# Kernel tuning notes

Measured on AMD Instinct MI355X. Metric: run time of the kernel, lower is better.

The kernel has to match this reference:

```python
import jax, jax.numpy as jnp
import numpy as np

ALPHA = 0.01  # LeakyReLU negative slope
NEG_INF = -1e12

def setup_inputs() -> dict:
    key = jax.random.key(0)
    k1, k2, k3, k4 = jax.random.split(key, 4)
    B, N, F_in, F_out = 8, 2048, 256, 128
    inp = jax.random.normal(k1, (B, N, F_in), dtype=jnp.float32)
    adj = jax.random.randint(k2, (B, N, N), 0, 2, dtype=jnp.int32)
    # xavier_uniform with gain=1.414
    limW = 1.414 * np.sqrt(6.0 / (F_in + F_out))
    W = jax.random.uniform(k3, (F_in, F_out), minval=-limW, maxval=limW, dtype=jnp.float32)
    lima = 1.414 * np.sqrt(6.0 / (2 * F_out + 1))
    a = jax.random.uniform(k4, (2 * F_out, 1), minval=-lima, maxval=lima, dtype=jnp.float32)
    return {"inp": inp, "adj": adj, "W": W, "a": a}

def reference(inp, adj, W, a):
    # h: [B, N, F_out]
    h = jnp.matmul(inp, W)
    F_out = W.shape[1]
    # Algebraic split of the attention vector: a = [a1; a2], so
    # e[b,i,j] = leakyrelu(h_i . a1 + h_j . a2)  -- avoids the O(N^2*2F) a_input.
    a1 = a[:F_out, 0]   # [F_out]
    a2 = a[F_out:, 0]   # [F_out]
    s1 = jnp.einsum('bnf,f->bn', h, a1)  # [B, N] source term
    s2 = jnp.einsum('bnf,f->bn', h, a2)  # [B, N] target term
    e = s1[:, :, None] + s2[:, None, :]  # [B, N, N]
    e = jnp.where(e > 0, e, ALPHA * e)   # leaky relu
    scores = jnp.where(adj > 0, e, NEG_INF)
    attention = jax.nn.softmax(scores, axis=2)  # [B, N, N]
    h_prime = jnp.matmul(attention, h)          # [B, N, F_out]
    return jax.nn.relu(h_prime)  # concat=True branch
```

## Files before the change

### kernel.cpp

```cpp
#include <hip/hip_runtime.h>
#include <hip/hip_bf16.h>

#define N_    2048
#define FIN   256
#define FOUT  128
#define ALPHA 0.01f
#define NEGINF -1000000000000.0f

typedef short bf16x8 __attribute__((ext_vector_type(8)));
typedef float f32x4  __attribute__((ext_vector_type(4)));

static __device__ __forceinline__ unsigned short f2bf(float x) {
    __hip_bfloat16 h = __float2bfloat16(x);
    return *reinterpret_cast<unsigned short*>(&h);
}

__global__ __launch_bounds__(256) void k_lin(
    const float* __restrict__ inp, const float* __restrict__ W,
    const float* __restrict__ av, __hip_bfloat16* __restrict__ hT,
    float* __restrict__ s1, float* __restrict__ s2)
{
    __shared__ float in_lds[32 * FIN];
    int g = blockIdx.x;
    int b = g & 7;
    int tile = g >> 3;
    int i0 = tile << 5;
    int t = threadIdx.x;

    const float4* src = reinterpret_cast<const float4*>(inp + ((size_t)(b * N_ + i0)) * FIN);
    float4* dst = reinterpret_cast<float4*>(in_lds);
#pragma unroll
    for (int c = 0; c < 8; ++c) dst[t + 256 * c] = src[t + 256 * c];
    __syncthreads();

    int fq = t & 31;
    int rg = t >> 5;
    float acc[4][4];
#pragma unroll
    for (int r = 0; r < 4; ++r)
#pragma unroll
        for (int j = 0; j < 4; ++j) acc[r][j] = 0.f;

    const float4* W4 = reinterpret_cast<const float4*>(W);
    for (int k = 0; k < FIN; k += 4) {
        float4 inr[4];
#pragma unroll
        for (int r = 0; r < 4; ++r)
            inr[r] = *reinterpret_cast<const float4*>(&in_lds[(rg * 4 + r) * FIN + k]);
#pragma unroll
        for (int kk = 0; kk < 4; ++kk) {
            float4 w4 = W4[(k + kk) * 32 + fq];
#pragma unroll
            for (int r = 0; r < 4; ++r) {
                float iv = (&inr[r].x)[kk];
                acc[r][0] = fmaf(iv, w4.x, acc[r][0]);
                acc[r][1] = fmaf(iv, w4.y, acc[r][1]);
                acc[r][2] = fmaf(iv, w4.z, acc[r][2]);
                acc[r][3] = fmaf(iv, w4.w, acc[r][3]);
            }
        }
    }

    float a1v[4], a2v[4];
#pragma unroll
    for (int j = 0; j < 4; ++j) {
        a1v[j] = av[fq * 4 + j];
        a2v[j] = av[FOUT + fq * 4 + j];
    }
#pragma unroll
    for (int r = 0; r < 4; ++r) {
        float p1 = acc[r][0] * a1v[0] + acc[r][1] * a1v[1] + acc[r][2] * a1v[2] + acc[r][3] * a1v[3];
        float p2 = acc[r][0] * a2v[0] + acc[r][1] * a2v[1] + acc[r][2] * a2v[2] + acc[r][3] * a2v[3];
#pragma unroll
        for (int off = 1; off < 32; off <<= 1) {
            p1 += __shfl_xor(p1, off);
            p2 += __shfl_xor(p2, off);
        }
        if (fq == 0) {
            int row = i0 + rg * 4 + r;
            s1[b * N_ + row] = p1;
            s2[b * N_ + row] = p2;
        }
    }

#pragma unroll
    for (int j = 0; j < 4; ++j) {
        ushort4 pk;
        pk.x = f2bf(acc[0][j]);
        pk.y = f2bf(acc[1][j]);
        pk.z = f2bf(acc[2][j]);
        pk.w = f2bf(acc[3][j]);
        *reinterpret_cast<ushort4*>(
            &hT[((size_t)(b * FOUT + fq * 4 + j)) * N_ + i0 + rg * 4]) = pk;
    }
}

__global__ __launch_bounds__(256, 4) void k_attn(
    const int* __restrict__ adj, const __hip_bfloat16* __restrict__ hT,
    const float* __restrict__ s1g, const float* __restrict__ s2g,
    float* __restrict__ out)
{
    __shared__ float m_s[4][16];
    __shared__ float l_s[4][16];
    __shared__ float L_s[16];
    __shared__ float accb[4][16][132];

    int g = blockIdx.x;
    int b = g & 7;
    int tile = g >> 3;
    int i0 = tile << 4;
    int t = threadIdx.x;
    int w = t >> 6;
    int l = t & 63;
    int r = l & 15;
    int lg = l >> 4;
    int jc = w * 512;

    const float s1r = s1g[b * N_ + i0 + r];
    size_t adj_off = ((size_t)(b * N_ + i0 + r)) * N_ + jc + lg * 8;
    const int4*   adjp = reinterpret_cast<const int4*>(adj + adj_off);
    const float4* s2p  = reinterpret_cast<const float4*>(s2g + b * N_ + jc + lg * 8);
    const bf16x8* hv   = reinterpret_cast<const bf16x8*>(hT);
    size_t h0 = (((size_t)(b * FOUT + r)) * N_ + jc + lg * 8) >> 3;
    const size_t FRAG_STRIDE = (size_t)16 * N_ / 8;

    float m_run = -3.0e38f;
    float l_run = 0.0f;
    f32x4 acc[8];
#pragma unroll
    for (int q = 0; q < 8; ++q) acc[q] = (f32x4){0.f, 0.f, 0.f, 0.f};

    for (int step = 0; step < 16; ++step) {
        int4 aj0 = adjp[step * 8];
        int4 aj1 = adjp[step * 8 + 1];
        float4 s2a = s2p[step * 8];
        float4 s2b = s2p[step * 8 + 1];

        float ev[8];
        ev[0] = s1r + s2a.x; ev[1] = s1r + s2a.y; ev[2] = s1r + s2a.z; ev[3] = s1r + s2a.w;
        ev[4] = s1r + s2b.x; ev[5] = s1r + s2b.y; ev[6] = s1r + s2b.z; ev[7] = s1r + s2b.w;
        int aji[8] = {aj0.x, aj0.y, aj0.z, aj0.w, aj1.x, aj1.y, aj1.z, aj1.w};
#pragma unroll
        for (int e = 0; e < 8; ++e) {
            float v = ev[e];
            v = fmaxf(v, ALPHA * v);
            ev[e] = (aji[e] > 0) ? v : NEGINF;
        }
        float mt = fmaxf(fmaxf(fmaxf(ev[0], ev[1]), fmaxf(ev[2], ev[3])),
                         fmaxf(fmaxf(ev[4], ev[5]), fmaxf(ev[6], ev[7])));
        mt = fmaxf(mt, __shfl_xor(mt, 16));
        mt = fmaxf(mt, __shfl_xor(mt, 32));

        if (__any(mt > m_run)) {
            float sc = (mt > m_run) ? __expf(m_run - mt) : 1.0f;
            m_run = fmaxf(m_run, mt);
            l_run *= sc;
            float sr0 = __shfl(sc, lg * 4 + 0);
            float sr1 = __shfl(sc, lg * 4 + 1);
            float sr2 = __shfl(sc, lg * 4 + 2);
            float sr3 = __shfl(sc, lg * 4 + 3);
            f32x4 srv = (f32x4){sr0, sr1, sr2, sr3};
#pragma unroll
            for (int q = 0; q < 8; ++q) acc[q] *= srv;
        }

        bf16x8 af;
        float ps = 0.f;
#pragma unroll
        for (int e = 0; e < 8; ++e) {
            float p = __expf(ev[e] - m_run);
            ps += p;
            af[e] = (short)f2bf(p);
        }
        l_run += ps;

#pragma unroll
        for (int q = 0; q < 8; ++q) {
            bf16x8 bfr = hv[h0 + (size_t)q * FRAG_STRIDE + step * 4];
            acc[q] = __builtin_amdgcn_mfma_f32_16x16x32_bf16(af, bfr, acc[q], 0, 0, 0);
        }
    }

    l_run += __shfl_xor(l_run, 16);
    l_run += __shfl_xor(l_run, 32);
    if (l < 16) { m_s[w][l] = m_run; l_s[w][l] = l_run; }
    __syncthreads();

    float mysc[4];
#pragma unroll
    for (int rr = 0; rr < 4; ++rr) {
        int ir = lg * 4 + rr;
        float M = fmaxf(fmaxf(m_s[0][ir], m_s[1][ir]), fmaxf(m_s[2][ir], m_s[3][ir]));
        float Ls = l_s[0][ir] * __expf(m_s[0][ir] - M)
                 + l_s[1][ir] * __expf(m_s[1][ir] - M)
                 + l_s[2][ir] * __expf(m_s[2][ir] - M)
                 + l_s[3][ir] * __expf(m_s[3][ir] - M);
        mysc[rr] = __expf(m_s[w][ir] - M);
        if (w == 0 && r == 0) L_s[ir] = Ls;
    }
#pragma unroll
    for (int q = 0; q < 8; ++q)
#pragma unroll
        for (int rr = 0; rr < 4; ++rr)
            accb[w][lg * 4 + rr][q * 16 + r] = acc[q][rr] * mysc[rr];
    __syncthreads();

    int f = t & 127;
    int rh = t >> 7;
#pragma unroll
    for (int rr = 0; rr < 8; ++rr) {
        int row = rh * 8 + rr;
        float v = accb[0][row][f] + accb[1][row][f] + accb[2][row][f] + accb[3][row][f];
        v = v / L_s[row];
        out[((size_t)(b * N_ + i0 + row)) * FOUT + f] = fmaxf(v, 0.f);
    }
}

extern "C" void kernel_launch(void* const* d_in, const int* in_sizes, int n_in,
                              void* d_out, int out_size, void* d_ws, size_t ws_size,
                              hipStream_t stream) {
    (void)in_sizes; (void)n_in; (void)out_size; (void)ws_size;
    const float* inp = (const float*)d_in[0];
    const int*   adj = (const int*)d_in[1];
    const float* W   = (const float*)d_in[2];
    const float* a   = (const float*)d_in[3];
    float* out = (float*)d_out;

    char* ws = (char*)d_ws;
    __hip_bfloat16* hT = (__hip_bfloat16*)ws;
    float* s1 = (float*)(ws + (size_t)8 * FOUT * N_ * 2);
    float* s2 = s1 + 8 * N_;

    k_lin<<<512, 256, 0, stream>>>(inp, W, a, hT, s1, s2);
    k_attn<<<1024, 256, 0, stream>>>(adj, hT, s1, s2, out);
}
```

Baseline: 284.4 us.

## Use precomputed per-row softmax bound instead of online max rescaling

Adds a small kernel that computes the per-batch maximum of s2. Because LeakyReLU is monotonic, leakyrelu(s1_i + max s2) bounds every score in row i, so the attention kernel drops the online max tracking, the accumulator rescaling and the cross-wave max merge. It also prefetches the next step's adj and s2 registers, and stages hT stores through LDS so the global writes are coalesced 32-byte chunks. The risk is accuracy: if the bound sits far above a row's real masked maximum, the exponentials can underflow. It also adds one extra kernel launch.

Result: no change. 286.6 us (+0.8%).

```diff
diff --git a/kernel.cpp b/kernel.cpp
--- a/kernel.cpp
+++ b/kernel.cpp
@@ -5,7 +5,6 @@
 #define FIN   256
 #define FOUT  128
 #define ALPHA 0.01f
-#define NEGINF -1000000000000.0f
 
 typedef short bf16x8 __attribute__((ext_vector_type(8)));
 typedef float f32x4  __attribute__((ext_vector_type(4)));
@@ -83,27 +82,49 @@
         }
     }
 
-#pragma unroll
-    for (int j = 0; j < 4; ++j) {
-        ushort4 pk;
-        pk.x = f2bf(acc[0][j]);
-        pk.y = f2bf(acc[1][j]);
-        pk.z = f2bf(acc[2][j]);
-        pk.w = f2bf(acc[3][j]);
-        *reinterpret_cast<ushort4*>(
-            &hT[((size_t)(b * FOUT + fq * 4 + j)) * N_ + i0 + rg * 4]) = pk;
-    }
+    __syncthreads();
+    unsigned short* hb = reinterpret_cast<unsigned short*>(in_lds);
+#pragma unroll
+    for (int j = 0; j < 4; ++j)
+#pragma unroll
+        for (int r = 0; r < 4; ++r)
+            hb[(fq * 4 + j) * 33 + rg * 4 + r] = f2bf(acc[r][j]);
+    __syncthreads();
+    {
+        int f = t >> 1;
+        int c0 = (t & 1) * 16;
+        unsigned short tmp[16];
+#pragma unroll
+        for (int c = 0; c < 16; ++c) tmp[c] = hb[f * 33 + c0 + c];
+        int4* dst4 = reinterpret_cast<int4*>(&hT[((size_t)(b * FOUT + f)) * N_ + i0 + c0]);
+        dst4[0] = reinterpret_cast<const int4*>(tmp)[0];
+        dst4[1] = reinterpret_cast<const int4*>(tmp)[1];
+    }
+}
+
+__global__ __launch_bounds__(256) void k_s2max(const float* __restrict__ s2,
+                                               float* __restrict__ s2max)
+{
+    __shared__ float red[4];
+    int b = blockIdx.x, t = threadIdx.x;
+    const float4* p = reinterpret_cast<const float4*>(s2 + b * N_);
+    float4 v0 = p[t], v1 = p[t + 256];
+    float m = fmaxf(fmaxf(fmaxf(v0.x, v0.y), fmaxf(v0.z, v0.w)),
+                    fmaxf(fmaxf(v1.x, v1.y), fmaxf(v1.z, v1.w)));
+#pragma unroll
+    for (int off = 1; off < 64; off <<= 1) m = fmaxf(m, __shfl_xor(m, off));
+    if ((t & 63) == 0) red[t >> 6] = m;
+    __syncthreads();
+    if (t == 0) s2max[b] = fmaxf(fmaxf(red[0], red[1]), fmaxf(red[2], red[3]));
 }
 
 __global__ __launch_bounds__(256, 4) void k_attn(
     const int* __restrict__ adj, const __hip_bfloat16* __restrict__ hT,
     const float* __restrict__ s1g, const float* __restrict__ s2g,
-    float* __restrict__ out)
+    const float* __restrict__ s2maxg, float* __restrict__ out)
 {
-    __shared__ float m_s[4][16];
+    __shared__ float accb[4][16][128];
     __shared__ float l_s[4][16];
-    __shared__ float L_s[16];
-    __shared__ float accb[4][16][132];
 
     int g = blockIdx.x;
     int b = g & 7;
@@ -117,58 +138,43 @@
     int jc = w * 512;
 
     const float s1r = s1g[b * N_ + i0 + r];
-    size_t adj_off = ((size_t)(b * N_ + i0 + r)) * N_ + jc + lg * 8;
-    const int4*   adjp = reinterpret_cast<const int4*>(adj + adj_off);
-    const float4* s2p  = reinterpret_cast<const float4*>(s2g + b * N_ + jc + lg * 8);
-    const bf16x8* hv   = reinterpret_cast<const bf16x8*>(hT);
+    float eb = s1r + s2maxg[b];
+    const float m_row = fmaxf(eb, ALPHA * eb);
+
+    const int4* adjp = reinterpret_cast<const int4*>(
+        adj + ((size_t)(b * N_ + i0 + r)) * N_ + jc + lg * 8);
+    const float4* s2p = reinterpret_cast<const float4*>(s2g + b * N_ + jc + lg * 8);
+    const bf16x8* hv = reinterpret_cast<const bf16x8*>(hT);
     size_t h0 = (((size_t)(b * FOUT + r)) * N_ + jc + lg * 8) >> 3;
-    const size_t FRAG_STRIDE = (size_t)16 * N_ / 8;
-
-    float m_run = -3.0e38f;
+    const size_t FRAG = (size_t)16 * N_ / 8;
+
     float l_run = 0.0f;
     f32x4 acc[8];
 #pragma unroll
     for (int q = 0; q < 8; ++q) acc[q] = (f32x4){0.f, 0.f, 0.f, 0.f};
 
+    int4 aj0 = adjp[0], aj1 = adjp[1];
+    float4 s2a = s2p[0], s2b = s2p[1];
+
     for (int step = 0; step < 16; ++step) {
-        int4 aj0 = adjp[step * 8];
-        int4 aj1 = adjp[step * 8 + 1];
-        float4 s2a = s2p[step * 8];
-        float4 s2b = s2p[step * 8 + 1];
-
-        float ev[8];
-        ev[0] = s1r + s2a.x; ev[1] = s1r + s2a.y; ev[2] = s1r + s2a.z; ev[3] = s1r + s2a.w;
-        ev[4] = s1r + s2b.x; ev[5] = s1r + s2b.y; ev[6] = s1r + s2b.z; ev[7] = s1r + s2b.w;
-        int aji[8] = {aj0.x, aj0.y, aj0.z, aj0.w, aj1.x, aj1.y, aj1.z, aj1.w};
-#pragma unroll
-        for (int e = 0; e < 8; ++e) {
-            float v = ev[e];
-            v = fmaxf(v, ALPHA * v);
-            ev[e] = (aji[e] > 0) ? v : NEGINF;
-        }
-        float mt = fmaxf(fmaxf(fmaxf(ev[0], ev[1]), fmaxf(ev[2], ev[3])),
-                         fmaxf(fmaxf(ev[4], ev[5]), fmaxf(ev[6], ev[7])));
-        mt = fmaxf(mt, __shfl_xor(mt, 16));
-        mt = fmaxf(mt, __shfl_xor(mt, 32));
-
-        if (__any(mt > m_run)) {
-            float sc = (mt > m_run) ? __expf(m_run - mt) : 1.0f;
-            m_run = fmaxf(m_run, mt);
-            l_run *= sc;
-            float sr0 = __shfl(sc, lg * 4 + 0);
-            float sr1 = __shfl(sc, lg * 4 + 1);
-            float sr2 = __shfl(sc, lg * 4 + 2);
-            float sr3 = __shfl(sc, lg * 4 + 3);
-            f32x4 srv = (f32x4){sr0, sr1, sr2, sr3};
-#pragma unroll
-            for (int q = 0; q < 8; ++q) acc[q] *= srv;
-        }
+        int4 c0 = aj0, c1 = aj1;
+        float4 ca = s2a, cb = s2b;
+        if (step < 15) {
+            aj0 = adjp[(step + 1) * 8];
+            aj1 = adjp[(step + 1) * 8 + 1];
+            s2a = s2p[(step + 1) * 8];
+            s2b = s2p[(step + 1) * 8 + 1];
+        }
+        float sv[8] = {ca.x, ca.y, ca.z, ca.w, cb.x, cb.y, cb.z, cb.w};
+        int am[8] = {c0.x, c0.y, c0.z, c0.w, c1.x, c1.y, c1.z, c1.w};
 
         bf16x8 af;
         float ps = 0.f;
 #pragma unroll
         for (int e = 0; e < 8; ++e) {
-            float p = __expf(ev[e] - m_run);
+            float v = s1r + sv[e];
+            v = fmaxf(v, ALPHA * v);
+            float p = (am[e] > 0) ? __expf(v - m_row) : 0.f;
             ps += p;
             af[e] = (short)f2bf(p);
         }
@@ -176,33 +182,20 @@
 
 #pragma unroll
         for (int q = 0; q < 8; ++q) {
-            bf16x8 bfr = hv[h0 + (size_t)q * FRAG_STRIDE + step * 4];
+            bf16x8 bfr = hv[h0 + (size_t)q * FRAG + step * 4];
             acc[q] = __builtin_amdgcn_mfma_f32_16x16x32_bf16(af, bfr, acc[q], 0, 0, 0);
         }
     }
 
     l_run += __shfl_xor(l_run, 16);
     l_run += __shfl_xor(l_run, 32);
-    if (l < 16) { m_s[w][l] = m_run; l_s[w][l] = l_run; }
-    __syncthreads();
-
-    float mysc[4];
-#pragma unroll
-    for (int rr = 0; rr < 4; ++rr) {
-        int ir = lg * 4 + rr;
-        float M = fmaxf(fmaxf(m_s[0][ir], m_s[1][ir]), fmaxf(m_s[2][ir], m_s[3][ir]));
-        float Ls = l_s[0][ir] * __expf(m_s[0][ir] - M)
-                 + l_s[1][ir] * __expf(m_s[1][ir] - M)
-                 + l_s[2][ir] * __expf(m_s[2][ir] - M)
-                 + l_s[3][ir] * __expf(m_s[3][ir] - M);
-        mysc[rr] = __expf(m_s[w][ir] - M);
-        if (w == 0 && r == 0) L_s[ir] = Ls;
-    }
+    if (l < 16) l_s[w][l] = l_run;
+
 #pragma unroll
     for (int q = 0; q < 8; ++q)
 #pragma unroll
         for (int rr = 0; rr < 4; ++rr)
-            accb[w][lg * 4 + rr][q * 16 + r] = acc[q][rr] * mysc[rr];
+            accb[w][lg * 4 + rr][q * 16 + r] = acc[q][rr];
     __syncthreads();
 
     int f = t & 127;
@@ -210,8 +203,9 @@
 #pragma unroll
     for (int rr = 0; rr < 8; ++rr) {
         int row = rh * 8 + rr;
+        float L = l_s[0][row] + l_s[1][row] + l_s[2][row] + l_s[3][row];
         float v = accb[0][row][f] + accb[1][row][f] + accb[2][row][f] + accb[3][row][f];
-        v = v / L_s[row];
+        v = v / L;
         out[((size_t)(b * N_ + i0 + row)) * FOUT + f] = fmaxf(v, 0.f);
     }
 }
@@ -230,7 +224,9 @@
     __hip_bfloat16* hT = (__hip_bfloat16*)ws;
     float* s1 = (float*)(ws + (size_t)8 * FOUT * N_ * 2);
     float* s2 = s1 + 8 * N_;
+    float* s2max = s2 + 8 * N_;
 
     k_lin<<<512, 256, 0, stream>>>(inp, W, a, hT, s1, s2);
-    k_attn<<<1024, 256, 0, stream>>>(adj, hT, s1, s2, out);
-}
+    k_s2max<<<8, 256, 0, stream>>>(s2, s2max);
+    k_attn<<<1024, 256, 0, stream>>>(adj, hT, s1, s2, s2max, out);
+}
```
